# Optimization experiments

Hardware: AMD Instinct MI355X
Metric: run time of the kernel (lower is better)

The kernel has to match this reference:

```python
import jax, jax.numpy as jnp
import numpy as np

T, B, S = 32, 64, 64          # tgt_len, batch, src_len
V, E, H, L = 32000, 512, 1024, 2  # vocab, word_vec, rnn_size, layers


def setup_inputs() -> dict:
    key = jax.random.key(0)
    ks = jax.random.split(key, 16)
    s = 0.02
    emb = jax.random.normal(ks[5], (V, E)) * s
    emb = emb.at[0].set(0.0)  # padding_idx=0 row is zero
    return {
        "input": jax.random.randint(ks[0], (T, B), 0, V),
        "h0": jax.random.normal(ks[1], (L, B, H)) * s,
        "c0": jax.random.normal(ks[2], (L, B, H)) * s,
        "context": jax.random.normal(ks[3], (S, B, H)),
        "init_output": jax.random.normal(ks[4], (B, H)) * s,
        "embedding": emb,
        "W_ih0": jax.random.normal(ks[6], (4 * H, E + H)) * s,  # layer0 input = emb + input-feed
        "W_hh0": jax.random.normal(ks[7], (4 * H, H)) * s,
        "b0": jnp.zeros((4 * H,), jnp.float32),
        "W_ih1": jax.random.normal(ks[8], (4 * H, H)) * s,
        "W_hh1": jax.random.normal(ks[9], (4 * H, H)) * s,
        "b1": jnp.zeros((4 * H,), jnp.float32),
        "attn_in_w": jax.random.normal(ks[10], (H, H)) * s,
        "attn_out_w": jax.random.normal(ks[11], (H, 2 * H)) * s,
        "copy_in_w": jax.random.normal(ks[12], (H, H)) * s,
    }


def _lstm_cell(x, h, c, W_ih, W_hh, b):
    g = x @ W_ih.T + h @ W_hh.T + b
    i, f, gg, o = jnp.split(g, 4, axis=-1)  # PyTorch gate order i,f,g,o
    c_new = jax.nn.sigmoid(f) * c + jax.nn.sigmoid(i) * jnp.tanh(gg)
    h_new = jax.nn.sigmoid(o) * jnp.tanh(c_new)
    return h_new, c_new


def _global_attention(in_w, out_w, query, ctx):
    # query: (B,H), ctx: (B,S,H)
    q = query @ in_w.T
    scores = jnp.einsum('bd,bsd->bs', q, ctx)
    a = jax.nn.softmax(scores, axis=-1)
    wctx = jnp.einsum('bs,bsd->bd', a, ctx)
    out = jnp.tanh(jnp.concatenate([wctx, query], axis=-1) @ out_w.T)
    return out, a


def reference(input, h0, c0, context, init_output, embedding,
              W_ih0, W_hh0, b0, W_ih1, W_hh1, b1,
              attn_in_w, attn_out_w, copy_in_w):
    ctx = jnp.transpose(context, (1, 0, 2))  # (B,S,H)
    emb = embedding[input]                    # (T,B,E)

    def step(carry, emb_t):
        h, c, out_feed = carry
        x = jnp.concatenate([emb_t, out_feed], axis=-1)  # input feed
        h0n, c0n = _lstm_cell(x, h[0], c[0], W_ih0, W_hh0, b0)
        h1n, c1n = _lstm_cell(h0n, h[1], c[1], W_ih1, W_hh1, b1)
        out, a_std = _global_attention(attn_in_w, attn_out_w, h1n, ctx)
        # copy attention: only the weights are kept by the original module
        qc = out @ copy_in_w.T
        a_copy = jax.nn.softmax(jnp.einsum('bd,bsd->bs', qc, ctx), axis=-1)
        new_carry = (jnp.stack([h0n, h1n]), jnp.stack([c0n, c1n]), out)
        return new_carry, (out, a_std, a_copy)

    (h_T, c_T, _), (outputs, attn_std, attn_copy) = jax.lax.scan(
        step, (h0, c0, init_output), emb)
    return outputs, (h_T, c_T), attn_std, attn_copy
```

## Files before the change

kernel.cpp:

```cpp
#include <hip/hip_runtime.h>

typedef unsigned short u16;
typedef unsigned int   u32;
typedef __attribute__((ext_vector_type(8))) __bf16 bfrag;
typedef __attribute__((ext_vector_type(4))) float  f32x4;
typedef __attribute__((ext_vector_type(2))) u32    u32x2;

#define DEVI static __device__ __forceinline__

#define ST4SC(p, v)    asm volatile("global_store_dword %0, %1, off sc0 sc1"  :: "v"(p), "v"(v) : "memory")
#define ST2SC(p, v)    asm volatile("global_store_short %0, %1, off sc0 sc1"  :: "v"(p), "v"(v) : "memory")
#define ST8SC(p, v)    asm volatile("global_store_dwordx2 %0, %1, off sc0 sc1" :: "v"(p), "v"(v) : "memory")
#define VMFLUSH()      asm volatile("s_waitcnt vmcnt(0)" ::: "memory")

constexpr long OUT_OFF = 0;
constexpr long HT_OFF  = 2097152;
constexpr long CT_OFF  = 2228224;
constexpr long AS_OFF  = 2359296;
constexpr long AC_OFF  = 2490368;

constexpr long WAO_O   = 0;
constexpr long WAI_O   = 4194304;
constexpr long WC_O    = 6291456;
constexpr long CTX_O   = 8388608;
constexpr long CTXW_O  = 16777216;
constexpr long CTXWC_O = 25165824;
constexpr long CTXOT_O = 33554432;
constexpr long EBF_O   = 41943040;
constexpr long OFF_O   = 44040192;
constexpr long HB0F_O  = 44302336;
constexpr long HB1F_O  = 44564480;
constexpr long ABUF_O  = 45875200;
constexpr long BAR_O   = 45891584;

constexpr int W0LDS_O = 0;
constexpr int W1LDS_O = 81920;
constexpr int SCR_O   = 147456;
constexpr int SCR2_O  = 156160;

struct KParams {
  const int* input; const float* h0; const float* c0; const float* context;
  const float* init_output; const float* embedding;
  const float* W_ih0; const float* W_hh0; const float* b0;
  const float* W_ih1; const float* W_hh1; const float* b1;
  const float* attn_in; const float* attn_out; const float* copy_in;
  float* out; char* ws;
};

DEVI float bf2f(u16 u) { u32 x = ((u32)u) << 16; return __builtin_bit_cast(float, x); }
DEVI u16 f2bf(float f) {
  u32 x = __builtin_bit_cast(u32, f);
  u32 r = x + 0x7fffu + ((x >> 16) & 1u);
  return (u16)(r >> 16);
}
DEVI void cvtc(const float* s, u16* d) {
  float4 v = *(const float4*)s;
  uint2 u;
  u.x = (u32)f2bf(v.x) | ((u32)f2bf(v.y) << 16);
  u.y = (u32)f2bf(v.z) | ((u32)f2bf(v.w) << 16);
  *(uint2*)d = u;
}
DEVI float sigm(float x)  { return 1.f / (1.f + __expf(-x)); }
DEVI float tanh_(float x) { return 1.f - 2.f / (__expf(2.f * x) + 1.f); }
DEVI f32x4 mfma16(bfrag a, bfrag b, f32x4 c) {
  return __builtin_amdgcn_mfma_f32_16x16x32_bf16(a, b, c, 0, 0, 0);
}
DEVI u32 fragoff(int m, int k) {
  return (u32)((((k >> 5) * 4 + (m >> 4)) * 64 + ((k >> 3) & 3) * 16 + (m & 15)) * 16 + (k & 7) * 2);
}

DEVI void pollflags(u32* flags, u32 gen) {
  int t = threadIdx.x;
  for (;;) {
    u32 a = __hip_atomic_load(&flags[t],       __ATOMIC_RELAXED, __HIP_MEMORY_SCOPE_AGENT);
    u32 b = __hip_atomic_load(&flags[64 + t],  __ATOMIC_RELAXED, __HIP_MEMORY_SCOPE_AGENT);
    u32 c = __hip_atomic_load(&flags[128 + t], __ATOMIC_RELAXED, __HIP_MEMORY_SCOPE_AGENT);
    u32 d = __hip_atomic_load(&flags[192 + t], __ATOMIC_RELAXED, __HIP_MEMORY_SCOPE_AGENT);
    if (__all((a >= gen) && (b >= gen) && (c >= gen) && (d >= gen))) break;
    __builtin_amdgcn_s_sleep(1);
  }
}
DEVI void barr_arrive(u32* flags, u32 gen) {
  VMFLUSH();
  __syncthreads();
  if (threadIdx.x == 0)
    __hip_atomic_store(&flags[blockIdx.x], gen, __ATOMIC_RELAXED, __HIP_MEMORY_SCOPE_AGENT);
}
DEVI void barr_wait(u32* flags, u32 gen) {
  if (threadIdx.x < 64) pollflags(flags, gen);
  __syncthreads();
  if (threadIdx.x == 0)
    __builtin_amdgcn_fence(__ATOMIC_ACQUIRE, "agent");
  __syncthreads();
  asm volatile("" ::: "memory");
}
DEVI void gsync_fence(u32* flags, u32 gen) {
  __syncthreads();
  if (threadIdx.x == 0) {
    __builtin_amdgcn_fence(__ATOMIC_RELEASE, "agent");
    __hip_atomic_store(&flags[blockIdx.x], gen, __ATOMIC_RELAXED, __HIP_MEMORY_SCOPE_AGENT);
  }
  if (threadIdx.x < 64) pollflags(flags, gen);
  if (threadIdx.x == 0) __builtin_amdgcn_fence(__ATOMIC_ACQUIRE, "agent");
  __syncthreads();
}

template<int N4>
DEVI void gseg(f32x4& acc, const char* Af, int kkA0, int mt, int lane,
               const char* W, int wRowK, int kkW0, int brow, int ke) {
  const u32 sw = (u32)((brow & 7) << 4);
#pragma unroll
  for (int g = 0; g < N4; ++g) {
#pragma unroll
    for (int q = 0; q < 4; ++q) {
      const char* pa = Af + ((((kkA0 + g * 4 + q) * 4 + mt) * 64 + lane) << 4);
      bfrag av = *(const bfrag*)pa;
      int kkW = kkW0 + g * 4 + q;
      u32 off = ((u32)(brow * wRowK + kkW * 32 + ke) * 2) ^ sw;
      acc = mfma16(av, *(const bfrag*)(W + off), acc);
    }
  }
}

DEVI void scr_store(float* scr, int slot, f32x4 acc) {
  const int lane = threadIdx.x & 63;
#pragma unroll
  for (int r = 0; r < 4; ++r)
    scr[slot * 272 + ((lane >> 4) * 4 + r) * 17 + (lane & 15)] = acc[r];
}

DEVI void pointwise64(int bid, const float* scr, const float* bias, float (&cst)[4], char* hfrag) {
  const int m = threadIdx.x;
  const int mt = m >> 4, ml = m & 15;
  u32 hp0 = 0, hp1 = 0;
#pragma unroll
  for (int u = 0; u < 4; ++u) {
    const int j = bid * 4 + u;
    float g0 = scr[(mt*2)*272 + ml*17 + u]      + scr[(mt*2+1)*272 + ml*17 + u]      + bias[j];
    float g1 = scr[(mt*2)*272 + ml*17 + 4 + u]  + scr[(mt*2+1)*272 + ml*17 + 4 + u]  + bias[1024 + j];
    float g2 = scr[(mt*2)*272 + ml*17 + 8 + u]  + scr[(mt*2+1)*272 + ml*17 + 8 + u]  + bias[2048 + j];
    float g3 = scr[(mt*2)*272 + ml*17 + 12 + u] + scr[(mt*2+1)*272 + ml*17 + 12 + u] + bias[3072 + j];
    float cn = sigm(g1) * cst[u] + sigm(g0) * tanh_(g2);
    cst[u] = cn;
    u32 hb = (u32)f2bf(sigm(g3) * tanh_(cn));
    if (u == 0) hp0 = hb; else if (u == 1) hp0 |= hb << 16;
    else if (u == 2) hp1 = hb; else hp1 |= hb << 16;
  }
  u32x2 v; v[0] = hp0; v[1] = hp1;
  ST8SC(hfrag + fragoff(m, bid * 4), v);
}

DEVI void ctxw_gemm(int mt, const u16* Ctx, const u16* Wm, u16* dst) {
  const int tid = threadIdx.x, lane = tid & 63, w = tid >> 6;
  const int arow = mt * 16 + (lane & 15);
  const int ke = (lane >> 4) * 8;
#pragma unroll
  for (int i = 0; i < 8; ++i) {
    int nt = w * 8 + i;
    const u16* A = Ctx + (long)arow * 1024 + ke;
    const u16* B = Wm + (long)(nt * 16 + (lane & 15)) * 1024 + ke;
    f32x4 acc = {0.f, 0.f, 0.f, 0.f};
    for (int kk = 0; kk < 1024; kk += 32)
      acc = mfma16(*(const bfrag*)(A + kk), *(const bfrag*)(B + kk), acc);
#pragma unroll
    for (int r = 0; r < 4; ++r)
      dst[(long)(mt * 16 + (lane >> 4) * 4 + r) * 1024 + nt * 16 + (lane & 15)] = f2bf(acc[r]);
  }
}

DEVI void ctxo_gemm(int bid, const u16* Ctx, const u16* Wao, u16* dst) {
  const int tid = threadIdx.x, lane = tid & 63, w = tid >> 6;
  const int arow = bid * 16 + (lane & 15);
  const int ke = (lane >> 4) * 8;
  const int b = bid >> 2, s0 = (bid & 3) * 16 + (lane >> 4) * 4;
#pragma unroll
  for (int i = 0; i < 8; ++i) {
    int nt = w * 8 + i;
    int j = nt * 16 + (lane & 15);
    const u16* A = Ctx + (long)arow * 1024 + ke;
    const u16* B = Wao + (long)j * 2048 + ke;
    f32x4 acc = {0.f, 0.f, 0.f, 0.f};
    for (int kk = 0; kk < 1024; kk += 32)
      acc = mfma16(*(const bfrag*)(A + kk), *(const bfrag*)(B + kk), acc);
    uint2 q;
    q.x = (u32)f2bf(acc[0]) | ((u32)f2bf(acc[1]) << 16);
    q.y = (u32)f2bf(acc[2]) | ((u32)f2bf(acc[3]) << 16);
    *(uint2*)(dst + ((long)(b * 1024 + j) * 64 + s0)) = q;
  }
}

__global__ __launch_bounds__(512, 1) void decoder_kernel(KParams p) {
  extern __shared__ char smem[];
  char*  W0   = smem + W0LDS_O;
  char*  W1   = smem + W1LDS_O;
  float* scr  = (float*)(smem + SCR_O);
  float* scr2 = (float*)(smem + SCR2_O);

  char* wsb = p.ws;
  u16* Wao   = (u16*)(wsb + WAO_O);
  u16* Wai   = (u16*)(wsb + WAI_O);
  u16* Wc    = (u16*)(wsb + WC_O);
  u16* Ctx   = (u16*)(wsb + CTX_O);
  u16* CtxW  = (u16*)(wsb + CTXW_O);
  u16* CtxWc = (u16*)(wsb + CTXWC_O);
  u16* CtxOT = (u16*)(wsb + CTXOT_O);
  u32* bar   = (u32*)(wsb + BAR_O);

  const int bid = blockIdx.x, tid = threadIdx.x;
  const int lane = tid & 63, w = tid >> 6;
  const long gtid = (long)bid * 512 + tid, NT = 256l * 512;
  u32 gen = 1;

  {
    float* tile = (float*)smem;
    for (int pass = 0; pass < 2; ++pass) {
      const float* src = pass ? p.copy_in : p.attn_in;
      u16* dst = pass ? Wc : Wai;
      int tr = bid >> 4, tc = bid & 15;
      {
        int r = tid >> 3, c = (tid & 7) * 8;
        const float4* s4 = (const float4*)(src + (long)(tr * 64 + r) * 1024 + tc * 64 + c);
        float4 a = s4[0], b = s4[1];
        float* tp = tile + r * 69 + c;
        tp[0] = a.x; tp[1] = a.y; tp[2] = a.z; tp[3] = a.w;
        tp[4] = b.x; tp[5] = b.y; tp[6] = b.z; tp[7] = b.w;
      }
      __syncthreads();
      {
        int r2 = tid >> 3, c2 = (tid & 7) * 8;
        u32 q[4];
#pragma unroll
        for (int i = 0; i < 4; ++i) {
          float lo = tile[(c2 + 2 * i) * 69 + r2];
          float hi = tile[(c2 + 2 * i + 1) * 69 + r2];
          q[i] = (u32)f2bf(lo) | ((u32)f2bf(hi) << 16);
        }
        *(uint4*)(dst + (long)(tc * 64 + r2) * 1024 + tr * 64 + c2) = *(uint4*)q;
      }
      __syncthreads();
    }
  }

  for (int i = tid; i < 5120; i += 512) {
    int row = i / 320, k = (i % 320) * 8;
    int R = (row >> 2) * 1024 + bid * 4 + (row & 3);
    const float* src = (k < 1536) ? (p.W_ih0 + (long)R * 1536 + k)
                                  : (p.W_hh0 + (long)R * 1024 + (k - 1536));
    float4 a = *(const float4*)src, b = *(const float4*)(src + 4);
    uint4 q;
    q.x = (u32)f2bf(a.x) | ((u32)f2bf(a.y) << 16);
    q.y = (u32)f2bf(a.z) | ((u32)f2bf(a.w) << 16);
    q.z = (u32)f2bf(b.x) | ((u32)f2bf(b.y) << 16);
    q.w = (u32)f2bf(b.z) | ((u32)f2bf(b.w) << 16);
    u32 off = ((u32)(row * 2560 + k) * 2) ^ ((u32)((row & 7) << 4));
    *(uint4*)(W0 + off) = q;
  }
  for (int i = tid; i < 4096; i += 512) {
    int row = i / 256, k = (i % 256) * 8;
    int R = (row >> 2) * 1024 + bid * 4 + (row & 3);
    const float* src = (k < 1024) ? (p.W_ih1 + (long)R * 1024 + k)
                                  : (p.W_hh1 + (long)R * 1024 + (k - 1024));
    float4 a = *(const float4*)src, b = *(const float4*)(src + 4);
    uint4 q;
    q.x = (u32)f2bf(a.x) | ((u32)f2bf(a.y) << 16);
    q.y = (u32)f2bf(a.z) | ((u32)f2bf(a.w) << 16);
    q.z = (u32)f2bf(b.x) | ((u32)f2bf(b.y) << 16);
    q.w = (u32)f2bf(b.z) | ((u32)f2bf(b.w) << 16);
    u32 off = ((u32)(row * 2048 + k) * 2) ^ ((u32)((row & 7) << 4));
    *(uint4*)(W1 + off) = q;
  }

  for (long i = gtid; i < 524288; i += NT) cvtc(p.attn_out + i * 4, Wao + i * 4);
  for (long i = gtid; i < 1048576; i += NT) {
    long b = i >> 14, s = (i >> 8) & 63, kq = i & 255;
    cvtc(p.context + ((s * 64 + b) * 1024 + kq * 4), Ctx + i * 4);
  }
  for (long i = gtid; i < 262144; i += NT) {
    long row = i >> 7; long t = row >> 6, b = row & 63;
    long k0 = (i & 127) * 4;
    long tok = p.input[row];
    cvtc(p.embedding + tok * 512 + k0,
         (u16*)(wsb + EBF_O + t * 65536 + fragoff((int)b, (int)k0)));
  }
  for (long i = gtid; i < 16384; i += NT) {
    long b = i >> 8, k0 = (i & 255) * 4;
    cvtc(p.init_output + i * 4, (u16*)(wsb + OFF_O + fragoff((int)b, (int)k0)));
  }
  for (long i = gtid; i < 32768; i += NT) {
    long l = i >> 14, rem = i & 16383, b = rem >> 8, k0 = (rem & 255) * 4;
    cvtc(p.h0 + i * 4,
         (u16*)(wsb + (l ? HB1F_O : HB0F_O) + 131072 + fragoff((int)b, (int)k0)));
  }

  float cR0[4] = {0.f, 0.f, 0.f, 0.f}, cR1[4] = {0.f, 0.f, 0.f, 0.f};
  if (tid < 64) {
#pragma unroll
    for (int u = 0; u < 4; ++u) {
      cR0[u] = p.c0[(long)tid * 1024 + bid * 4 + u];
      cR1[u] = p.c0[65536 + (long)tid * 1024 + bid * 4 + u];
    }
  }

  gsync_fence(bar, gen); ++gen;

  ctxw_gemm(bid, Ctx, Wai, CtxW);
  ctxw_gemm(bid, Ctx, Wc, CtxWc);
  ctxo_gemm(bid, Ctx, Wao, CtxOT);
  gsync_fence(bar, gen); ++gen;

  const int xcd = bid & 7, idx = bid >> 3;
  const int ntP4 = xcd * 8 + (idx & 7), mtP4 = idx >> 3;
  const int browP4 = ntP4 * 16 + (lane & 15);
  const int ke_ = (lane >> 4) * 8;
  bfrag waoreg[4];
#pragma unroll
  for (int q = 0; q < 4; ++q)
    waoreg[q] = *(const bfrag*)(Wao + (long)browP4 * 2048 + 1024 + (w * 4 + q) * 32 + ke_);

  const int mt_ = w & 3, kh_ = w >> 2;
  const int brow_ = lane & 15;

  f32x4 accP1 = {0.f, 0.f, 0.f, 0.f}, accP2;
  {
    const char* E0  = wsb + EBF_O;
    const char* H0p = wsb + HB0F_O + 131072;
    if (kh_ == 0) {
      gseg<2>(accP1, E0,  0,  mt_, lane, W0, 2560, 0,  brow_, ke_);
      gseg<4>(accP1, H0p, 0,  mt_, lane, W0, 2560, 48, brow_, ke_);
    } else {
      gseg<2>(accP1, E0,  8,  mt_, lane, W0, 2560, 8,  brow_, ke_);
      gseg<4>(accP1, H0p, 16, mt_, lane, W0, 2560, 64, brow_, ke_);
    }
  }

  for (int t = 0; t < 32; ++t) {
    const int cur = t & 1, prev = cur ^ 1;
    const char* OFc   = wsb + OFF_O  + (long)cur  * 131072;
    char*       Hb0cF = wsb + HB0F_O + (long)cur  * 131072;
    char*       Hb1cF = wsb + HB1F_O + (long)cur  * 131072;
    const char* Hb1pF = wsb + HB1F_O + (long)prev * 131072;

    {
      f32x4 acc = accP1;
      if (kh_ == 0) gseg<4>(acc, OFc, 0,  mt_, lane, W0, 2560, 16, brow_, ke_);
      else          gseg<4>(acc, OFc, 16, mt_, lane, W0, 2560, 32, brow_, ke_);
      scr_store(scr, mt_ * 2 + kh_, acc);
      __syncthreads();
      if (tid < 64) pointwise64(bid, scr, p.b0, cR0, Hb0cF);
    }
    barr_arrive(bar, gen);
    accP2 = f32x4{0.f, 0.f, 0.f, 0.f};
    if (kh_ == 0) gseg<4>(accP2, Hb1pF, 0,  mt_, lane, W1, 2048, 32, brow_, ke_);
    else          gseg<4>(accP2, Hb1pF, 16, mt_, lane, W1, 2048, 48, brow_, ke_);
    barr_wait(bar, gen); ++gen;

    {
      f32x4 acc = accP2;
      if (kh_ == 0) gseg<4>(acc, Hb0cF, 0,  mt_, lane, W1, 2048, 0,  brow_, ke_);
      else          gseg<4>(acc, Hb0cF, 16, mt_, lane, W1, 2048, 16, brow_, ke_);
      scr_store(scr, mt_ * 2 + kh_, acc);
      __syncthreads();
      if (tid < 64) pointwise64(bid, scr, p.b1, cR1, Hb1cF);
    }
    barr_arrive(bar, gen);
    accP1 = f32x4{0.f, 0.f, 0.f, 0.f};
    {
      const char* En = wsb + EBF_O + (long)((t + 1) & 31) * 65536;
      if (kh_ == 0) {
        gseg<2>(accP1, En,    0,  mt_, lane, W0, 2560, 0,  brow_, ke_);
        gseg<2>(accP1, Hb0cF, 0,  mt_, lane, W0, 2560, 48, brow_, ke_);
      } else {
        gseg<2>(accP1, En,    8,  mt_, lane, W0, 2560, 8,  brow_, ke_);
        gseg<2>(accP1, Hb0cF, 16, mt_, lane, W0, 2560, 64, brow_, ke_);
      }
    }
    barr_wait(bar, gen); ++gen;

    if (bid < 64) {
      const int b = bid;
      float h1v[16];
      {
        int k0 = lane * 16;
        const u32* hp0 = (const u32*)(Hb1cF + fragoff(b, k0));
        const u32* hp1 = (const u32*)(Hb1cF + fragoff(b, k0 + 8));
        u32 uu[8] = {hp0[0], hp0[1], hp0[2], hp0[3], hp1[0], hp1[1], hp1[2], hp1[3]};
#pragma unroll
        for (int i = 0; i < 8; ++i) {
          h1v[2 * i]     = bf2f((u16)(uu[i] & 0xffff));
          h1v[2 * i + 1] = bf2f((u16)(uu[i] >> 16));
        }
      }
      const u16* cwb = CtxW + (long)b * 65536;
#pragma unroll
      for (int si = 0; si < 8; ++si) {
        int s = w * 8 + si;
        const u32* u = (const u32*)(cwb + (long)s * 1024 + lane * 16);
        float acc = 0.f;
#pragma unroll
        for (int i = 0; i < 8; ++i) {
          u32 x = u[i];
          acc += h1v[2 * i] * bf2f((u16)(x & 0xffff));
          acc += h1v[2 * i + 1] * bf2f((u16)(x >> 16));
        }
#pragma unroll
        for (int off = 32; off; off >>= 1) acc += __shfl_down(acc, off, 64);
        if (lane == 0) scr2[s] = acc;
      }
      __syncthreads();
      if (w == 0) {
        float v = scr2[lane];
        float mx = v;
#pragma unroll
        for (int off = 32; off; off >>= 1) mx = fmaxf(mx, __shfl_xor(mx, off, 64));
        float e = __expf(v - mx);
        float sm = e;
#pragma unroll
        for (int off = 32; off; off >>= 1) sm += __shfl_xor(sm, off, 64);
        float a = e / sm;
        ST4SC(wsb + ABUF_O + (u32)(b * 64 + lane) * 4, __builtin_bit_cast(u32, a));
        ST4SC((char*)(p.out + AS_OFF + (long)t * 4096 + b * 64 + lane), __builtin_bit_cast(u32, a));
      }
    }
    {
      const char* bp = Hb1cF;
      bfrag h0_ = *(const bfrag*)(bp + ((((w * 4 + 0) * 4 + mtP4) * 64 + lane) << 4));
      bfrag h1_ = *(const bfrag*)(bp + ((((w * 4 + 1) * 4 + mtP4) * 64 + lane) << 4));
      bfrag h2_ = *(const bfrag*)(bp + ((((w * 4 + 2) * 4 + mtP4) * 64 + lane) << 4));
      bfrag h3_ = *(const bfrag*)(bp + ((((w * 4 + 3) * 4 + mtP4) * 64 + lane) << 4));
      f32x4 a4 = {0.f, 0.f, 0.f, 0.f};
      a4 = mfma16(h0_, waoreg[0], a4);
      a4 = mfma16(h1_, waoreg[1], a4);
      a4 = mfma16(h2_, waoreg[2], a4);
      a4 = mfma16(h3_, waoreg[3], a4);
      scr_store(scr, w, a4);
    }
    barr_arrive(bar, gen);
    if (kh_ == 0) gseg<2>(accP1, Hb0cF, 8,  mt_, lane, W0, 2560, 56, brow_, ke_);
    else          gseg<2>(accP1, Hb0cF, 24, mt_, lane, W0, 2560, 72, brow_, ke_);
    barr_wait(bar, gen); ++gen;

    {
      {
        int b0i = tid >> 6, s0i = tid & 63;
        int b1i = (tid + 512) >> 6;
        scr2[tid]       = *(const float*)(wsb + ABUF_O + (u32)(((mtP4 * 16 + b0i) * 64 + s0i)) * 4);
        scr2[tid + 512] = *(const float*)(wsb + ABUF_O + (u32)(((mtP4 * 16 + b1i) * 64 + s0i)) * 4);
      }
      __syncthreads();
      const int pair = tid >> 1, half = tid & 1;
      const int m_l = pair >> 4, j_l = pair & 15;
      const int b = mtP4 * 16 + m_l, j = ntP4 * 16 + j_l;
      const u32* cp = (const u32*)(CtxOT + ((long)(b * 1024 + j) * 64 + half * 32));
      const float* al = scr2 + m_l * 64 + half * 32;
      float acc = 0.f;
#pragma unroll
      for (int i = 0; i < 16; ++i) {
        u32 x = cp[i];
        acc += al[2 * i] * bf2f((u16)(x & 0xffff));
        acc += al[2 * i + 1] * bf2f((u16)(x >> 16));
      }
      float v = acc + __shfl_xor(acc, 1, 64);
      if (half == 0) {
        float h1p = 0.f;
#pragma unroll
        for (int q = 0; q < 8; ++q) h1p += scr[q * 272 + m_l * 17 + j_l];
        v = tanh_(v + h1p);
        ST4SC((char*)(p.out + (long)t * 65536 + b * 1024 + j), __builtin_bit_cast(u32, v));
        u32 hv = (u32)f2bf(v);
        ST2SC(wsb + OFF_O + (long)((t + 1) & 1) * 131072 + fragoff(b, j), hv);
      }
    }
    barr_arrive(bar, gen);
    barr_wait(bar, gen); ++gen;
  }

  if (tid < 64) {
#pragma unroll
    for (int u = 0; u < 4; ++u) {
      int j = bid * 4 + u;
      p.out[CT_OFF + (long)tid * 1024 + j]         = cR0[u];
      p.out[CT_OFF + 65536 + (long)tid * 1024 + j] = cR1[u];
    }
  }
  if (tid < 256) {
    int u = tid >> 6, m = tid & 63, j = bid * 4 + u;
    u16 a0 = *(const u16*)(wsb + HB0F_O + 131072 + fragoff(m, j));
    u16 a1 = *(const u16*)(wsb + HB1F_O + 131072 + fragoff(m, j));
    p.out[HT_OFF + (long)m * 1024 + j]         = bf2f(a0);
    p.out[HT_OFF + 65536 + (long)m * 1024 + j] = bf2f(a1);
  }

  if (bid < 64) {
    const int b = bid;
    u16* cw = (u16*)smem;
    __syncthreads();
    {
      const uint4* src = (const uint4*)(CtxWc + (long)b * 65536);
      uint4* dst = (uint4*)cw;
      for (int i = tid; i < 8192; i += 512) dst[i] = src[i];
    }
    __syncthreads();
    float* lds_s = scr;
    for (int t = 0; t < 32; ++t) {
      float ov[16];
      {
        const float4* op = (const float4*)(p.out + (long)t * 65536 + b * 1024 + lane * 16);
#pragma unroll
        for (int i = 0; i < 4; ++i) {
          float4 v = op[i];
          ov[4 * i] = v.x; ov[4 * i + 1] = v.y; ov[4 * i + 2] = v.z; ov[4 * i + 3] = v.w;
        }
      }
#pragma unroll
      for (int si = 0; si < 8; ++si) {
        int s = w * 8 + si;
        const u32* u = (const u32*)(cw + s * 1024 + lane * 16);
        float acc = 0.f;
#pragma unroll
        for (int i = 0; i < 8; ++i) {
          u32 x = u[i];
          acc += ov[2 * i] * bf2f((u16)(x & 0xffff));
          acc += ov[2 * i + 1] * bf2f((u16)(x >> 16));
        }
#pragma unroll
        for (int off = 32; off; off >>= 1) acc += __shfl_down(acc, off, 64);
        if (lane == 0) lds_s[s] = acc;
      }
      __syncthreads();
      if (w == 0) {
        float v = lds_s[lane];
        float mx = v;
#pragma unroll
        for (int off = 32; off; off >>= 1) mx = fmaxf(mx, __shfl_xor(mx, off, 64));
        float e = __expf(v - mx);
        float sm = e;
#pragma unroll
        for (int off = 32; off; off >>= 1) sm += __shfl_xor(sm, off, 64);
        p.out[AC_OFF + (long)t * 4096 + b * 64 + lane] = e / sm;
      }
      __syncthreads();
    }
  }
}

extern "C" void kernel_launch(void* const* d_in, const int* in_sizes, int n_in,
                              void* d_out, int out_size, void* d_ws, size_t ws_size,
                              hipStream_t stream) {
  KParams p;
  p.input       = (const int*)d_in[0];
  p.h0          = (const float*)d_in[1];
  p.c0          = (const float*)d_in[2];
  p.context     = (const float*)d_in[3];
  p.init_output = (const float*)d_in[4];
  p.embedding   = (const float*)d_in[5];
  p.W_ih0       = (const float*)d_in[6];
  p.W_hh0       = (const float*)d_in[7];
  p.b0          = (const float*)d_in[8];
  p.W_ih1       = (const float*)d_in[9];
  p.W_hh1       = (const float*)d_in[10];
  p.b1          = (const float*)d_in[11];
  p.attn_in     = (const float*)d_in[12];
  p.attn_out    = (const float*)d_in[13];
  p.copy_in     = (const float*)d_in[14];
  p.out         = (float*)d_out;
  p.ws          = (char*)d_ws;

  (void)hipFuncSetAttribute((const void*)decoder_kernel,
                            hipFuncAttributeMaxDynamicSharedMemorySize, 160256);
  (void)hipMemsetAsync((char*)d_ws + BAR_O, 0, 2048, stream);
  void* args[] = { &p };
  (void)hipLaunchCooperativeKernel((void*)decoder_kernel, dim3(256), dim3(512),
                                   args, 160256, stream);
}
```

Before: 1.885 ms.

## Use per-timestep buffers and sc stores to drop acquire fences from grid barriers

Replaces the double-buffered hidden, input-feed and attention buffers with per-timestep slots, so no address is ever rewritten and stale-cache hazards go away. All cross-block producer stores become system-coherent sc0 sc1 stores. That allows the agent-scope acquire fence and extra __syncthreads to be removed from every grid barrier wait, and the fenced init barriers become plain arrive/wait. This costs more workspace memory and relies on the bypass stores plus fresh addresses for correctness without explicit fences.

After: 1.679 ms. 1.12x faster.

```diff
diff --git a/kernel.cpp b/kernel.cpp
--- a/kernel.cpp
+++ b/kernel.cpp
@@ -5,12 +5,14 @@
 typedef __attribute__((ext_vector_type(8))) __bf16 bfrag;
 typedef __attribute__((ext_vector_type(4))) float  f32x4;
 typedef __attribute__((ext_vector_type(2))) u32    u32x2;
+typedef __attribute__((ext_vector_type(4))) u32    u32x4;
 
 #define DEVI static __device__ __forceinline__
 
-#define ST4SC(p, v)    asm volatile("global_store_dword %0, %1, off sc0 sc1"  :: "v"(p), "v"(v) : "memory")
-#define ST2SC(p, v)    asm volatile("global_store_short %0, %1, off sc0 sc1"  :: "v"(p), "v"(v) : "memory")
+#define ST2SC(p, v)    asm volatile("global_store_short %0, %1, off sc0 sc1"   :: "v"(p), "v"(v) : "memory")
+#define ST4SC(p, v)    asm volatile("global_store_dword %0, %1, off sc0 sc1"   :: "v"(p), "v"(v) : "memory")
 #define ST8SC(p, v)    asm volatile("global_store_dwordx2 %0, %1, off sc0 sc1" :: "v"(p), "v"(v) : "memory")
+#define ST16SC(p, v)   asm volatile("global_store_dwordx4 %0, %1, off sc0 sc1" :: "v"(p), "v"(v) : "memory")
 #define VMFLUSH()      asm volatile("s_waitcnt vmcnt(0)" ::: "memory")
 
 constexpr long OUT_OFF = 0;
@@ -20,18 +22,21 @@
 constexpr long AC_OFF  = 2490368;
 
 constexpr long WAO_O   = 0;
-constexpr long WAI_O   = 4194304;
-constexpr long WC_O    = 6291456;
-constexpr long CTX_O   = 8388608;
+constexpr long CTX_O   = 4194304;
+constexpr long OFR_O   = 0;
+constexpr long H0R_O   = 4194304;
+constexpr long H1R_O   = 8388608;
+constexpr long WAI_O   = 12582912;
+constexpr long WC_O    = 14680064;
 constexpr long CTXW_O  = 16777216;
 constexpr long CTXWC_O = 25165824;
 constexpr long CTXOT_O = 33554432;
 constexpr long EBF_O   = 41943040;
-constexpr long OFF_O   = 44040192;
-constexpr long HB0F_O  = 44302336;
-constexpr long HB1F_O  = 44564480;
-constexpr long ABUF_O  = 45875200;
-constexpr long BAR_O   = 45891584;
+constexpr long OF0_O   = 44040192;
+constexpr long H00_O   = 44171264;
+constexpr long H10_O   = 44302336;
+constexpr long AB_O    = 44433408;
+constexpr long BAR_O   = 44957696;
 
 constexpr int W0LDS_O = 0;
 constexpr int W1LDS_O = 81920;
@@ -53,12 +58,12 @@
   u32 r = x + 0x7fffu + ((x >> 16) & 1u);
   return (u16)(r >> 16);
 }
-DEVI void cvtc(const float* s, u16* d) {
+DEVI void cvtc_sc(const float* s, char* d) {
   float4 v = *(const float4*)s;
-  uint2 u;
-  u.x = (u32)f2bf(v.x) | ((u32)f2bf(v.y) << 16);
-  u.y = (u32)f2bf(v.z) | ((u32)f2bf(v.w) << 16);
-  *(uint2*)d = u;
+  u32x2 u;
+  u[0] = (u32)f2bf(v.x) | ((u32)f2bf(v.y) << 16);
+  u[1] = (u32)f2bf(v.z) | ((u32)f2bf(v.w) << 16);
+  ST8SC(d, u);
 }
 DEVI float sigm(float x)  { return 1.f / (1.f + __expf(-x)); }
 DEVI float tanh_(float x) { return 1.f - 2.f / (__expf(2.f * x) + 1.f); }
@@ -68,6 +73,9 @@
 DEVI u32 fragoff(int m, int k) {
   return (u32)((((k >> 5) * 4 + (m >> 4)) * 64 + ((k >> 3) & 3) * 16 + (m & 15)) * 16 + (k & 7) * 2);
 }
+DEVI char* of_slot(char* w, int s) { return w + (s ? OFR_O + (long)(s - 1) * 131072 : OF0_O); }
+DEVI char* h0_slot(char* w, int s) { return w + (s ? H0R_O + (long)(s - 1) * 131072 : H00_O); }
+DEVI char* h1_slot(char* w, int s) { return w + (s ? H1R_O + (long)(s - 1) * 131072 : H10_O); }
 
 DEVI void pollflags(u32* flags, u32 gen) {
   int t = threadIdx.x;
@@ -89,20 +97,7 @@
 DEVI void barr_wait(u32* flags, u32 gen) {
   if (threadIdx.x < 64) pollflags(flags, gen);
   __syncthreads();
-  if (threadIdx.x == 0)
-    __builtin_amdgcn_fence(__ATOMIC_ACQUIRE, "agent");
-  __syncthreads();
   asm volatile("" ::: "memory");
-}
-DEVI void gsync_fence(u32* flags, u32 gen) {
-  __syncthreads();
-  if (threadIdx.x == 0) {
-    __builtin_amdgcn_fence(__ATOMIC_RELEASE, "agent");
-    __hip_atomic_store(&flags[blockIdx.x], gen, __ATOMIC_RELAXED, __HIP_MEMORY_SCOPE_AGENT);
-  }
-  if (threadIdx.x < 64) pollflags(flags, gen);
-  if (threadIdx.x == 0) __builtin_amdgcn_fence(__ATOMIC_ACQUIRE, "agent");
-  __syncthreads();
 }
 
 template<int N4>
@@ -164,7 +159,8 @@
       acc = mfma16(*(const bfrag*)(A + kk), *(const bfrag*)(B + kk), acc);
 #pragma unroll
     for (int r = 0; r < 4; ++r)
-      dst[(long)(mt * 16 + (lane >> 4) * 4 + r) * 1024 + nt * 16 + (lane & 15)] = f2bf(acc[r]);
+      ST2SC((char*)(dst + (long)(mt * 16 + (lane >> 4) * 4 + r) * 1024 + nt * 16 + (lane & 15)),
+            (u32)f2bf(acc[r]));
   }
 }
 
@@ -182,10 +178,10 @@
     f32x4 acc = {0.f, 0.f, 0.f, 0.f};
     for (int kk = 0; kk < 1024; kk += 32)
       acc = mfma16(*(const bfrag*)(A + kk), *(const bfrag*)(B + kk), acc);
-    uint2 q;
-    q.x = (u32)f2bf(acc[0]) | ((u32)f2bf(acc[1]) << 16);
-    q.y = (u32)f2bf(acc[2]) | ((u32)f2bf(acc[3]) << 16);
-    *(uint2*)(dst + ((long)(b * 1024 + j) * 64 + s0)) = q;
+    u32x2 q;
+    q[0] = (u32)f2bf(acc[0]) | ((u32)f2bf(acc[1]) << 16);
+    q[1] = (u32)f2bf(acc[2]) | ((u32)f2bf(acc[3]) << 16);
+    ST8SC((char*)(dst + ((long)(b * 1024 + j) * 64 + s0)), q);
   }
 }
 
@@ -228,14 +224,14 @@
       __syncthreads();
       {
         int r2 = tid >> 3, c2 = (tid & 7) * 8;
-        u32 q[4];
+        u32x4 q;
 #pragma unroll
         for (int i = 0; i < 4; ++i) {
           float lo = tile[(c2 + 2 * i) * 69 + r2];
           float hi = tile[(c2 + 2 * i + 1) * 69 + r2];
           q[i] = (u32)f2bf(lo) | ((u32)f2bf(hi) << 16);
         }
-        *(uint4*)(dst + (long)(tc * 64 + r2) * 1024 + tr * 64 + c2) = *(uint4*)q;
+        ST16SC((char*)(dst + (long)(tc * 64 + r2) * 1024 + tr * 64 + c2), q);
       }
       __syncthreads();
     }
@@ -270,26 +266,24 @@
     *(uint4*)(W1 + off) = q;
   }
 
-  for (long i = gtid; i < 524288; i += NT) cvtc(p.attn_out + i * 4, Wao + i * 4);
+  for (long i = gtid; i < 524288; i += NT) cvtc_sc(p.attn_out + i * 4, (char*)(Wao + i * 4));
   for (long i = gtid; i < 1048576; i += NT) {
     long b = i >> 14, s = (i >> 8) & 63, kq = i & 255;
-    cvtc(p.context + ((s * 64 + b) * 1024 + kq * 4), Ctx + i * 4);
+    cvtc_sc(p.context + ((s * 64 + b) * 1024 + kq * 4), (char*)(Ctx + i * 4));
   }
   for (long i = gtid; i < 262144; i += NT) {
     long row = i >> 7; long t = row >> 6, b = row & 63;
     long k0 = (i & 127) * 4;
     long tok = p.input[row];
-    cvtc(p.embedding + tok * 512 + k0,
-         (u16*)(wsb + EBF_O + t * 65536 + fragoff((int)b, (int)k0)));
+    cvtc_sc(p.embedding + tok * 512 + k0, wsb + EBF_O + t * 65536 + fragoff((int)b, (int)k0));
   }
   for (long i = gtid; i < 16384; i += NT) {
     long b = i >> 8, k0 = (i & 255) * 4;
-    cvtc(p.init_output + i * 4, (u16*)(wsb + OFF_O + fragoff((int)b, (int)k0)));
+    cvtc_sc(p.init_output + i * 4, of_slot(wsb, 0) + fragoff((int)b, (int)k0));
   }
   for (long i = gtid; i < 32768; i += NT) {
     long l = i >> 14, rem = i & 16383, b = rem >> 8, k0 = (rem & 255) * 4;
-    cvtc(p.h0 + i * 4,
-         (u16*)(wsb + (l ? HB1F_O : HB0F_O) + 131072 + fragoff((int)b, (int)k0)));
+    cvtc_sc(p.h0 + i * 4, (l ? h1_slot(wsb, 0) : h0_slot(wsb, 0)) + fragoff((int)b, (int)k0));
   }
 
   float cR0[4] = {0.f, 0.f, 0.f, 0.f}, cR1[4] = {0.f, 0.f, 0.f, 0.f};
@@ -301,12 +295,12 @@
     }
   }
 
-  gsync_fence(bar, gen); ++gen;
+  barr_arrive(bar, gen); barr_wait(bar, gen); ++gen;
 
   ctxw_gemm(bid, Ctx, Wai, CtxW);
   ctxw_gemm(bid, Ctx, Wc, CtxWc);
   ctxo_gemm(bid, Ctx, Wao, CtxOT);
-  gsync_fence(bar, gen); ++gen;
+  barr_arrive(bar, gen); barr_wait(bar, gen); ++gen;
 
   const int xcd = bid & 7, idx = bid >> 3;
   const int ntP4 = xcd * 8 + (idx & 7), mtP4 = idx >> 3;
@@ -323,7 +317,7 @@
   f32x4 accP1 = {0.f, 0.f, 0.f, 0.f}, accP2;
   {
     const char* E0  = wsb + EBF_O;
-    const char* H0p = wsb + HB0F_O + 131072;
+    const char* H0p = h0_slot(wsb, 0);
     if (kh_ == 0) {
       gseg<2>(accP1, E0,  0,  mt_, lane, W0, 2560, 0,  brow_, ke_);
       gseg<4>(accP1, H0p, 0,  mt_, lane, W0, 2560, 48, brow_, ke_);
@@ -334,11 +328,11 @@
   }
 
   for (int t = 0; t < 32; ++t) {
-    const int cur = t & 1, prev = cur ^ 1;
-    const char* OFc   = wsb + OFF_O  + (long)cur  * 131072;
-    char*       Hb0cF = wsb + HB0F_O + (long)cur  * 131072;
-    char*       Hb1cF = wsb + HB1F_O + (long)cur  * 131072;
-    const char* Hb1pF = wsb + HB1F_O + (long)prev * 131072;
+    const char* OFc   = of_slot(wsb, t);
+    char*       Hb0cF = h0_slot(wsb, t + 1);
+    char*       Hb1cF = h1_slot(wsb, t + 1);
+    const char* Hb1pF = h1_slot(wsb, t);
+    char*       ABt   = wsb + AB_O + (long)t * 16384;
 
     {
       f32x4 acc = accP1;
@@ -417,7 +411,7 @@
 #pragma unroll
         for (int off = 32; off; off >>= 1) sm += __shfl_xor(sm, off, 64);
         float a = e / sm;
-        ST4SC(wsb + ABUF_O + (u32)(b * 64 + lane) * 4, __builtin_bit_cast(u32, a));
+        ST4SC(ABt + (u32)(b * 64 + lane) * 4, __builtin_bit_cast(u32, a));
         ST4SC((char*)(p.out + AS_OFF + (long)t * 4096 + b * 64 + lane), __builtin_bit_cast(u32, a));
       }
     }
@@ -443,8 +437,8 @@
       {
         int b0i = tid >> 6, s0i = tid & 63;
         int b1i = (tid + 512) >> 6;
-        scr2[tid]       = *(const float*)(wsb + ABUF_O + (u32)(((mtP4 * 16 + b0i) * 64 + s0i)) * 4);
-        scr2[tid + 512] = *(const float*)(wsb + ABUF_O + (u32)(((mtP4 * 16 + b1i) * 64 + s0i)) * 4);
+        scr2[tid]       = *(const float*)(ABt + (u32)(((mtP4 * 16 + b0i) * 64 + s0i)) * 4);
+        scr2[tid + 512] = *(const float*)(ABt + (u32)(((mtP4 * 16 + b1i) * 64 + s0i)) * 4);
       }
       __syncthreads();
       const int pair = tid >> 1, half = tid & 1;
@@ -467,7 +461,7 @@
         v = tanh_(v + h1p);
         ST4SC((char*)(p.out + (long)t * 65536 + b * 1024 + j), __builtin_bit_cast(u32, v));
         u32 hv = (u32)f2bf(v);
-        ST2SC(wsb + OFF_O + (long)((t + 1) & 1) * 131072 + fragoff(b, j), hv);
+        ST2SC(of_slot(wsb, t + 1) + fragoff(b, j), hv);
       }
     }
     barr_arrive(bar, gen);
@@ -484,8 +478,8 @@
   }
   if (tid < 256) {
     int u = tid >> 6, m = tid & 63, j = bid * 4 + u;
-    u16 a0 = *(const u16*)(wsb + HB0F_O + 131072 + fragoff(m, j));
-    u16 a1 = *(const u16*)(wsb + HB1F_O + 131072 + fragoff(m, j));
+    u16 a0 = *(const u16*)(h0_slot(wsb, 32) + fragoff(m, j));
+    u16 a1 = *(const u16*)(h1_slot(wsb, 32) + fragoff(m, j));
     p.out[HT_OFF + (long)m * 1024 + j]         = bf2f(a0);
     p.out[HT_OFF + 65536 + (long)m * 1024 + j] = bf2f(a1);
   }
```
